# Performance work log

Hardware: AMD Instinct MI355X
Metric: run time of the kernel (lower is better)

Reference implementation:

```python
import jax, jax.numpy as jnp
import numpy as np

N = 16384          # num nodes (128 graphs x 128 turbines)
E = 262144         # edges before self loops
TURBINE_NUM = 128
D_IN = 512         # input_dim (= 2*hidden_dim1)
H1 = 256           # hidden_dim1
H2 = 256           # hidden_dim2
NEG_SLOPE = 0.2    # PyG GATConv default leaky relu slope


def _glorot(key, shape, fan_in):
    return jax.random.normal(key, shape, dtype=jnp.float32) / np.sqrt(fan_in)


def setup_inputs() -> dict:
    key = jax.random.key(0)
    ks = jax.random.split(key, 12)
    x = jax.random.normal(ks[0], (N, H2), dtype=jnp.float32)
    adj = jax.random.randint(ks[1], (2, E), 0, N, dtype=jnp.int64)
    # fc: Linear(hidden_dim2 -> hidden_dim1); stored as [in, out]
    W_fc = _glorot(ks[2], (H2, H1), H2)
    b_fc = jnp.zeros((H1,), dtype=jnp.float32)
    # gat1: GATConv(H1 -> H1, heads=2, concat)
    W1 = _glorot(ks[3], (H1, 2 * H1), H1)
    a1_src = _glorot(ks[4], (2, H1), H1)
    a1_dst = _glorot(ks[5], (2, H1), H1)
    b1 = jnp.zeros((2 * H1,), dtype=jnp.float32)
    # gat2: GATConv(D_IN -> D_IN, heads=1, concat)
    W2 = _glorot(ks[6], (D_IN, D_IN), D_IN)
    a2_src = _glorot(ks[7], (1, D_IN), D_IN)
    a2_dst = _glorot(ks[8], (1, D_IN), D_IN)
    b2 = jnp.zeros((D_IN,), dtype=jnp.float32)
    return dict(x=x, adj=adj, W_fc=W_fc, b_fc=b_fc, W1=W1, a1_src=a1_src,
                a1_dst=a1_dst, b1=b1, W2=W2, a2_src=a2_src, a2_dst=a2_dst, b2=b2)


def gat_conv(x, src, dst, W, a_src, a_dst, bias, heads, out_ch):
    """PyG GATConv (eval mode, self loops already in src/dst)."""
    n = x.shape[0]
    h = (x @ W).reshape(n, heads, out_ch)                 # [N,H,C]
    al_s = jnp.einsum('nhc,hc->nh', h, a_src)             # [N,H]
    al_d = jnp.einsum('nhc,hc->nh', h, a_dst)
    e = jax.nn.leaky_relu(al_s[src] + al_d[dst], NEG_SLOPE)  # [E,H]
    # segment softmax over incoming edges per destination node
    e_max = jax.ops.segment_max(e, dst, num_segments=n)
    e_exp = jnp.exp(e - e_max[dst])
    denom = jax.ops.segment_sum(e_exp, dst, num_segments=n)
    alpha = e_exp / (denom[dst] + 1e-16)                  # [E,H]
    msg = h[src] * alpha[:, :, None]                      # [E,H,C]
    out = jax.ops.segment_sum(msg, dst, num_segments=n)   # [N,H,C]
    return out.reshape(n, heads * out_ch) + bias


def reference(x, adj, W_fc, b_fc, W1, a1_src, a1_dst, b1, W2, a2_src, a2_dst, b2):
    # add self loops (PyG GATConv default)
    loops = jnp.arange(N, dtype=adj.dtype)
    src = jnp.concatenate([adj[0], loops])
    dst = jnp.concatenate([adj[1], loops])
    h = jax.nn.relu(x @ W_fc + b_fc)                      # fc + ReLU
    h = gat_conv(h, src, dst, W1, a1_src, a1_dst, b1, heads=2, out_ch=H1)
    h = jax.nn.relu(h)
    h = gat_conv(h, src, dst, W2, a2_src, a2_dst, b2, heads=1, out_ch=D_IN)
    y = jax.nn.relu(h)
    return y.reshape(-1, TURBINE_NUM, y.shape[1])         # [128,128,512]
```

## Files before the change

kernel.cpp:

```cpp
#include <hip/hip_runtime.h>

#define N_NODES 16384
#define N_EDGES 262144
#define E_TOT   (N_EDGES + N_NODES)
#define NEG_SLOPE 0.2f

typedef __attribute__((ext_vector_type(8))) short short8;
typedef __attribute__((ext_vector_type(4))) float floatx4;
typedef __attribute__((ext_vector_type(4))) int intx4;

__device__ __forceinline__ float bf2f(ushort u) {
    return __uint_as_float(((unsigned)u) << 16);
}
__device__ __forceinline__ ushort f2bf(float f) {
    unsigned u = __float_as_uint(f);
    u += 0x7fffu + ((u >> 16) & 1u);
    return (ushort)(u >> 16);
}
__device__ __forceinline__ float leaky(float x) {
    return x > 0.f ? x : NEG_SLOPE * x;
}

#define PREP_CAST   524288
#define PREP_T0     (PREP_CAST)
#define PREP_T1     (PREP_T0 + 65536)
#define PREP_T2     (PREP_T1 + 131072)
#define PREP_Z      (PREP_T2 + 262144)
#define PREP_TOT    (PREP_Z + 4096)

__global__ __launch_bounds__(256) void k_prep(const float* __restrict__ x,
                                              ushort* __restrict__ xb,
                                              const float* __restrict__ Wfc,
                                              ushort* __restrict__ WfcT,
                                              const float* __restrict__ W1,
                                              ushort* __restrict__ W1T,
                                              const float* __restrict__ W2,
                                              ushort* __restrict__ W2T,
                                              int* __restrict__ counts) {
    int idx = blockIdx.x * 256 + threadIdx.x;
    if (idx < PREP_CAST) {
        floatx4 v0 = *(const floatx4*)(x + (size_t)idx * 8);
        floatx4 v1 = *(const floatx4*)(x + (size_t)idx * 8 + 4);
        short8 r;
        r[0] = (short)f2bf(v0[0]); r[1] = (short)f2bf(v0[1]);
        r[2] = (short)f2bf(v0[2]); r[3] = (short)f2bf(v0[3]);
        r[4] = (short)f2bf(v1[0]); r[5] = (short)f2bf(v1[1]);
        r[6] = (short)f2bf(v1[2]); r[7] = (short)f2bf(v1[3]);
        *(short8*)(xb + (size_t)idx * 8) = r;
    } else if (idx < PREP_T1) {
        int t = idx - PREP_T0;
        int k = t >> 8, n = t & 255;
        WfcT[n * 256 + k] = f2bf(Wfc[t]);
    } else if (idx < PREP_T2) {
        int t = idx - PREP_T1;
        int k = t >> 9, n = t & 511;
        W1T[n * 256 + k] = f2bf(W1[t]);
    } else if (idx < PREP_Z) {
        int t = idx - PREP_T2;
        int k = t >> 9, n = t & 511;
        W2T[n * 512 + k] = f2bf(W2[t]);
    } else if (idx < PREP_TOT) {
        int t = idx - PREP_Z;
        *(intx4*)(counts + t * 4) = (intx4){0, 0, 0, 0};
    }
}

__global__ __launch_bounds__(256) void k_hist(const int* __restrict__ adj,
                                              int* __restrict__ counts) {
    int e = blockIdx.x * 256 + threadIdx.x;
    if (e < E_TOT) {
        int d = (e < N_EDGES) ? adj[N_EDGES + e] : (e - N_EDGES);
        atomicAdd(&counts[d], 1);
    }
}

__global__ __launch_bounds__(1024) void k_scan(const int* __restrict__ counts,
                                               int* __restrict__ offs,
                                               int* __restrict__ cursor) {
    __shared__ int wsum[16];
    int t = threadIdx.x, lane = t & 63, w = t >> 6;
    int local[16];
    int tot = 0;
#pragma unroll
    for (int i = 0; i < 16; i++) {
        local[i] = tot;
        tot += counts[t * 16 + i];
    }
    int incl = tot;
#pragma unroll
    for (int d = 1; d < 64; d <<= 1) {
        int v = __shfl_up(incl, d, 64);
        if (lane >= d) incl += v;
    }
    if (lane == 63) wsum[w] = incl;
    __syncthreads();
    if (w == 0) {
        int v = (lane < 16) ? wsum[lane] : 0;
#pragma unroll
        for (int d = 1; d < 16; d <<= 1) {
            int u = __shfl_up(v, d, 64);
            if (lane >= d) v += u;
        }
        if (lane < 16) wsum[lane] = v;
    }
    __syncthreads();
    int base = ((w == 0) ? 0 : wsum[w - 1]) + incl - tot;
#pragma unroll
    for (int i = 0; i < 16; i++) {
        int o = base + local[i];
        offs[t * 16 + i] = o;
        cursor[t * 16 + i] = o;
    }
    if (t == 1023) offs[N_NODES] = wsum[15];
}

__global__ __launch_bounds__(256) void k_scatter(const int* __restrict__ adj,
                                                 int* __restrict__ cursor,
                                                 int* __restrict__ esrc) {
    int e = blockIdx.x * 256 + threadIdx.x;
    if (e < E_TOT) {
        int s, d;
        if (e < N_EDGES) { s = adj[e]; d = adj[N_EDGES + e]; }
        else             { s = e - N_EDGES; d = s; }
        int pos = atomicAdd(&cursor[d], 1);
        esrc[pos] = s;
    }
}

#define GM 128
#define GN 128
#define GK 64
#define LDK2 72

__global__ __launch_bounds__(256) void gemm128(const ushort* __restrict__ A,
                                               const ushort* __restrict__ BT,
                                               const float* __restrict__ bias,
                                               ushort* __restrict__ C,
                                               int M, int Nc, int K, int relu) {
    __shared__ ushort As[GM * LDK2];
    __shared__ ushort Bs[GN * LDK2];
    int tid = threadIdx.x, wave = tid >> 6, lane = tid & 63;
    int quad = lane >> 4, l16 = lane & 15;
    int bm = blockIdx.x * GM, bn = blockIdx.y * GN;
    int wm = (wave & 1) * 64, wn = (wave >> 1) * 64;

    floatx4 acc[4][4];
#pragma unroll
    for (int mi = 0; mi < 4; mi++)
#pragma unroll
        for (int ni = 0; ni < 4; ni++)
            acc[mi][ni] = (floatx4){0.f, 0.f, 0.f, 0.f};

    for (int kb = 0; kb < K; kb += GK) {
        short8 av[4], bv[4];
#pragma unroll
        for (int t = 0; t < 4; t++) {
            int ci = tid + 256 * t;
            int row = ci >> 3, col = (ci & 7) * 8;
            av[t] = *(const short8*)(A + (size_t)(bm + row) * K + kb + col);
            bv[t] = *(const short8*)(BT + (size_t)(bn + row) * K + kb + col);
        }
        __syncthreads();
#pragma unroll
        for (int t = 0; t < 4; t++) {
            int ci = tid + 256 * t;
            int row = ci >> 3, col = (ci & 7) * 8;
            *(short8*)&As[row * LDK2 + col] = av[t];
            *(short8*)&Bs[row * LDK2 + col] = bv[t];
        }
        __syncthreads();

#pragma unroll
        for (int kk = 0; kk < GK; kk += 32) {
            short8 af[4], bf[4];
#pragma unroll
            for (int mi = 0; mi < 4; mi++)
                af[mi] = *(const short8*)&As[(wm + mi * 16 + l16) * LDK2 + kk + quad * 8];
#pragma unroll
            for (int ni = 0; ni < 4; ni++)
                bf[ni] = *(const short8*)&Bs[(wn + ni * 16 + l16) * LDK2 + kk + quad * 8];
#pragma unroll
            for (int mi = 0; mi < 4; mi++)
#pragma unroll
                for (int ni = 0; ni < 4; ni++)
                    acc[mi][ni] = __builtin_amdgcn_mfma_f32_16x16x32_bf16(
                        af[mi], bf[ni], acc[mi][ni], 0, 0, 0);
        }
    }

#pragma unroll
    for (int mi = 0; mi < 4; mi++) {
        int row = bm + wm + mi * 16 + quad * 4;
#pragma unroll
        for (int ni = 0; ni < 4; ni++) {
            int col = bn + wn + ni * 16 + l16;
            float bv = bias ? bias[col] : 0.f;
#pragma unroll
            for (int i = 0; i < 4; i++) {
                float v = acc[mi][ni][i] + bv;
                if (relu) v = fmaxf(v, 0.f);
                C[(size_t)(row + i) * Nc + col] = f2bf(v);
            }
        }
    }
}

__global__ __launch_bounds__(256) void k_dots(const ushort* __restrict__ h,
                                              const float* __restrict__ asrc,
                                              const float* __restrict__ adst,
                                              float* __restrict__ als,
                                              float* __restrict__ ald,
                                              int heads) {
    int wave = threadIdx.x >> 6, lane = threadIdx.x & 63;
    int n = blockIdx.x * 4 + wave;
    const ushort* hr = h + (size_t)n * 512;
    int c = lane * 8;
    short8 hv = *(const short8*)(hr + c);
    floatx4 s0 = *(const floatx4*)(asrc + c);
    floatx4 s1 = *(const floatx4*)(asrc + c + 4);
    floatx4 d0 = *(const floatx4*)(adst + c);
    floatx4 d1 = *(const floatx4*)(adst + c + 4);
    float ps = 0.f, pd = 0.f;
#pragma unroll
    for (int j = 0; j < 4; j++) {
        float hf0 = bf2f((ushort)hv[j]);
        float hf1 = bf2f((ushort)hv[j + 4]);
        ps += hf0 * s0[j] + hf1 * s1[j];
        pd += hf0 * d0[j] + hf1 * d1[j];
    }
    int w = (heads == 2) ? 32 : 64;
    for (int m = 1; m < w; m <<= 1) {
        ps += __shfl_xor(ps, m, 64);
        pd += __shfl_xor(pd, m, 64);
    }
    if (heads == 2) {
        if (lane == 0)  { als[n * 2]     = ps; ald[n * 2]     = pd; }
        if (lane == 32) { als[n * 2 + 1] = ps; ald[n * 2 + 1] = pd; }
    } else {
        if (lane == 0)  { als[n] = ps; ald[n] = pd; }
    }
}

__global__ __launch_bounds__(256) void k_agg(const ushort* __restrict__ h,
                                             const float* __restrict__ als,
                                             const float* __restrict__ ald,
                                             const int* __restrict__ offs,
                                             const int* __restrict__ esrc,
                                             const float* __restrict__ bias,
                                             ushort* __restrict__ outb,
                                             float* __restrict__ outf,
                                             int heads) {
    int wave = threadIdx.x >> 6, lane = threadIdx.x & 63;
    int n = blockIdx.x * 4 + wave;
    int base = offs[n];
    int deg  = offs[n + 1] - base;

    int myhead = (heads == 2) ? (lane >> 5) : 0;
    int c = (heads == 2) ? (myhead * 256 + (lane & 31) * 8) : lane * 8;

    float aldh0 = ald[n * heads];
    float aldh1 = (heads == 2) ? ald[n * heads + 1] : 0.f;

    float m0 = -1e30f, m1 = -1e30f;
    for (int cb = 0; cb < deg; cb += 64) {
        int i = cb + lane;
        if (i < deg) {
            int s = esrc[base + i];
            m0 = fmaxf(m0, leaky(als[s * heads] + aldh0));
            if (heads == 2) m1 = fmaxf(m1, leaky(als[s * 2 + 1] + aldh1));
        }
    }
#pragma unroll
    for (int msk = 1; msk < 64; msk <<= 1) {
        m0 = fmaxf(m0, __shfl_xor(m0, msk, 64));
        m1 = fmaxf(m1, __shfl_xor(m1, msk, 64));
    }

    float s0 = 0.f, s1 = 0.f;
    for (int cb = 0; cb < deg; cb += 64) {
        int i = cb + lane;
        if (i < deg) {
            int s = esrc[base + i];
            s0 += __expf(leaky(als[s * heads] + aldh0) - m0);
            if (heads == 2) s1 += __expf(leaky(als[s * 2 + 1] + aldh1) - m1);
        }
    }
#pragma unroll
    for (int msk = 1; msk < 64; msk <<= 1) {
        s0 += __shfl_xor(s0, msk, 64);
        s1 += __shfl_xor(s1, msk, 64);
    }
    float inv0 = 1.f / (s0 + 1e-16f);
    float inv1 = 1.f / (s1 + 1e-16f);

    float acc[8];
#pragma unroll
    for (int q = 0; q < 8; q++) acc[q] = 0.f;
    const ushort* hc = h + c;

    for (int cb = 0; cb < deg; cb += 64) {
        int i = cb + lane;
        int sv = 0;
        float p0 = 0.f, p1 = 0.f;
        if (i < deg) {
            sv = esrc[base + i];
            p0 = __expf(leaky(als[sv * heads] + aldh0) - m0) * inv0;
            if (heads == 2) p1 = __expf(leaky(als[sv * 2 + 1] + aldh1) - m1) * inv1;
        }
        int cnt = min(64, deg - cb);
        int j = 0;
        for (; j + 4 <= cnt; j += 4) {
            int sj0 = __shfl(sv, j, 64);
            int sj1 = __shfl(sv, j + 1, 64);
            int sj2 = __shfl(sv, j + 2, 64);
            int sj3 = __shfl(sv, j + 3, 64);
            float a00 = __shfl(p0, j, 64),     a01 = __shfl(p1, j, 64);
            float a10 = __shfl(p0, j + 1, 64), a11 = __shfl(p1, j + 1, 64);
            float a20 = __shfl(p0, j + 2, 64), a21 = __shfl(p1, j + 2, 64);
            float a30 = __shfl(p0, j + 3, 64), a31 = __shfl(p1, j + 3, 64);
            float al0 = myhead ? a01 : a00;
            float al1 = myhead ? a11 : a10;
            float al2 = myhead ? a21 : a20;
            float al3 = myhead ? a31 : a30;
            short8 h0v = *(const short8*)(hc + (size_t)sj0 * 512);
            short8 h1v = *(const short8*)(hc + (size_t)sj1 * 512);
            short8 h2v = *(const short8*)(hc + (size_t)sj2 * 512);
            short8 h3v = *(const short8*)(hc + (size_t)sj3 * 512);
#pragma unroll
            for (int q = 0; q < 8; q++) {
                acc[q] += al0 * bf2f((ushort)h0v[q]);
                acc[q] += al1 * bf2f((ushort)h1v[q]);
                acc[q] += al2 * bf2f((ushort)h2v[q]);
                acc[q] += al3 * bf2f((ushort)h3v[q]);
            }
        }
        for (; j < cnt; j++) {
            int s = __shfl(sv, j, 64);
            float a0 = __shfl(p0, j, 64), a1 = __shfl(p1, j, 64);
            float al = myhead ? a1 : a0;
            short8 hv = *(const short8*)(hc + (size_t)s * 512);
#pragma unroll
            for (int q = 0; q < 8; q++) acc[q] += al * bf2f((ushort)hv[q]);
        }
    }

    float v[8];
#pragma unroll
    for (int q = 0; q < 8; q++) v[q] = fmaxf(acc[q] + bias[c + q], 0.f);
    if (outf) {
        float* op = outf + (size_t)n * 512 + c;
        *(floatx4*)op       = (floatx4){v[0], v[1], v[2], v[3]};
        *(floatx4*)(op + 4) = (floatx4){v[4], v[5], v[6], v[7]};
    } else {
        short8 r;
#pragma unroll
        for (int q = 0; q < 8; q++) r[q] = (short)f2bf(v[q]);
        *(short8*)(outb + (size_t)n * 512 + c) = r;
    }
}

extern "C" void kernel_launch(void* const* d_in, const int* in_sizes, int n_in,
                              void* d_out, int out_size, void* d_ws, size_t ws_size,
                              hipStream_t stream) {
    const float* x   = (const float*)d_in[0];
    const int*   adj = (const int*)d_in[1];
    const float* Wfc = (const float*)d_in[2];
    const float* bfc = (const float*)d_in[3];
    const float* W1  = (const float*)d_in[4];
    const float* a1s = (const float*)d_in[5];
    const float* a1d = (const float*)d_in[6];
    const float* b1  = (const float*)d_in[7];
    const float* W2  = (const float*)d_in[8];
    const float* a2s = (const float*)d_in[9];
    const float* a2d = (const float*)d_in[10];
    const float* b2  = (const float*)d_in[11];
    float* out = (float*)d_out;

    char* ws = (char*)d_ws;
    size_t off = 0;
    auto alloc = [&](size_t bytes) -> void* {
        void* p = ws + off;
        off += (bytes + 255) & ~(size_t)255;
        return p;
    };
    ushort* xb   = (ushort*)alloc((size_t)N_NODES * 256 * 2);
    ushort* h0b  = (ushort*)alloc((size_t)N_NODES * 256 * 2);
    ushort* h1b  = (ushort*)alloc((size_t)N_NODES * 512 * 2);
    ushort* g1b  = (ushort*)alloc((size_t)N_NODES * 512 * 2);
    int* counts  = (int*)alloc(N_NODES * 4);
    int* offs    = (int*)alloc((N_NODES + 1) * 4);
    int* cursor  = (int*)alloc(N_NODES * 4);
    int* esrc    = (int*)alloc(E_TOT * 4);
    ushort* WfcT = (ushort*)alloc(256 * 256 * 2);
    ushort* W1T  = (ushort*)alloc(512 * 256 * 2);
    ushort* W2T  = (ushort*)alloc(512 * 512 * 2);
    float* als1  = (float*)alloc(N_NODES * 2 * 4);
    float* ald1  = (float*)alloc(N_NODES * 2 * 4);
    float* als2  = (float*)alloc(N_NODES * 4);
    float* ald2  = (float*)alloc(N_NODES * 4);

    k_prep<<<PREP_TOT / 256, 256, 0, stream>>>(x, xb, Wfc, WfcT, W1, W1T, W2, W2T,
                                               counts);

    k_hist<<<(E_TOT + 255) / 256, 256, 0, stream>>>(adj, counts);
    k_scan<<<1, 1024, 0, stream>>>(counts, offs, cursor);
    k_scatter<<<(E_TOT + 255) / 256, 256, 0, stream>>>(adj, cursor, esrc);

    gemm128<<<dim3(N_NODES / GM, 256 / GN), 256, 0, stream>>>(xb, WfcT, bfc, h0b,
                                                              N_NODES, 256, 256, 1);
    gemm128<<<dim3(N_NODES / GM, 512 / GN), 256, 0, stream>>>(h0b, W1T, nullptr, h1b,
                                                              N_NODES, 512, 256, 0);
    k_dots<<<N_NODES / 4, 256, 0, stream>>>(h1b, a1s, a1d, als1, ald1, 2);
    k_agg<<<N_NODES / 4, 256, 0, stream>>>(h1b, als1, ald1, offs, esrc, b1,
                                           g1b, nullptr, 2);

    gemm128<<<dim3(N_NODES / GM, 512 / GN), 256, 0, stream>>>(g1b, W2T, nullptr, h1b,
                                                              N_NODES, 512, 512, 0);
    k_dots<<<N_NODES / 4, 256, 0, stream>>>(h1b, a2s, a2d, als2, ald2, 1);
    k_agg<<<N_NODES / 4, 256, 0, stream>>>(h1b, als2, ald2, offs, esrc, b2,
                                           nullptr, out, 1);
}
```

Baseline: 263.1 us.

## Split GAT aggregation across two waves per node and use direct-to-LDS GEMM loads

The aggregation kernel now assigns two waves to each destination node. Each wave gathers alternating edges, and the partial sums are combined through shared memory, which increases memory-level parallelism for the gather. The GEMM replaces register-staged global-to-LDS copies with global_load_lds into an unpadded tile and adds a trailing barrier. The cost is that the softmax max and sum passes are duplicated per wave, and the unpadded LDS layout may cause bank conflicts.

```diff
diff --git a/kernel.cpp b/kernel.cpp
--- a/kernel.cpp
+++ b/kernel.cpp
@@ -19,6 +19,12 @@
 }
 __device__ __forceinline__ float leaky(float x) {
     return x > 0.f ? x : NEG_SLOPE * x;
+}
+
+__device__ __forceinline__ void load_lds16(const void* g, void* l) {
+    __builtin_amdgcn_global_load_lds(
+        (const __attribute__((address_space(1))) unsigned int*)g,
+        (__attribute__((address_space(3))) unsigned int*)l, 16, 0, 0);
 }
 
 #define PREP_CAST   524288
@@ -130,15 +136,14 @@
 #define GM 128
 #define GN 128
 #define GK 64
-#define LDK2 72
 
 __global__ __launch_bounds__(256) void gemm128(const ushort* __restrict__ A,
                                                const ushort* __restrict__ BT,
                                                const float* __restrict__ bias,
                                                ushort* __restrict__ C,
                                                int M, int Nc, int K, int relu) {
-    __shared__ ushort As[GM * LDK2];
-    __shared__ ushort Bs[GN * LDK2];
+    __shared__ ushort As[GM * GK];
+    __shared__ ushort Bs[GN * GK];
     int tid = threadIdx.x, wave = tid >> 6, lane = tid & 63;
     int quad = lane >> 4, l16 = lane & 15;
     int bm = blockIdx.x * GM, bn = blockIdx.y * GN;
@@ -151,22 +156,18 @@
         for (int ni = 0; ni < 4; ni++)
             acc[mi][ni] = (floatx4){0.f, 0.f, 0.f, 0.f};
 
+    int lrow = lane >> 3;
+    int lcol = (lane & 7) * 8;
+    const ushort* pA = A + (size_t)(bm + wave * 32 + lrow) * K + lcol;
+    const ushort* pB = BT + (size_t)(bn + wave * 32 + lrow) * K + lcol;
+    ushort* lA = &As[(wave * 32) * GK];
+    ushort* lB = &Bs[(wave * 32) * GK];
+
     for (int kb = 0; kb < K; kb += GK) {
-        short8 av[4], bv[4];
 #pragma unroll
         for (int t = 0; t < 4; t++) {
-            int ci = tid + 256 * t;
-            int row = ci >> 3, col = (ci & 7) * 8;
-            av[t] = *(const short8*)(A + (size_t)(bm + row) * K + kb + col);
-            bv[t] = *(const short8*)(BT + (size_t)(bn + row) * K + kb + col);
-        }
-        __syncthreads();
-#pragma unroll
-        for (int t = 0; t < 4; t++) {
-            int ci = tid + 256 * t;
-            int row = ci >> 3, col = (ci & 7) * 8;
-            *(short8*)&As[row * LDK2 + col] = av[t];
-            *(short8*)&Bs[row * LDK2 + col] = bv[t];
+            load_lds16(pA + (size_t)(t * 8) * K + kb, lA + t * 8 * GK);
+            load_lds16(pB + (size_t)(t * 8) * K + kb, lB + t * 8 * GK);
         }
         __syncthreads();
 
@@ -175,10 +176,10 @@
             short8 af[4], bf[4];
 #pragma unroll
             for (int mi = 0; mi < 4; mi++)
-                af[mi] = *(const short8*)&As[(wm + mi * 16 + l16) * LDK2 + kk + quad * 8];
+                af[mi] = *(const short8*)&As[(wm + mi * 16 + l16) * GK + kk + quad * 8];
 #pragma unroll
             for (int ni = 0; ni < 4; ni++)
-                bf[ni] = *(const short8*)&Bs[(wn + ni * 16 + l16) * LDK2 + kk + quad * 8];
+                bf[ni] = *(const short8*)&Bs[(wn + ni * 16 + l16) * GK + kk + quad * 8];
 #pragma unroll
             for (int mi = 0; mi < 4; mi++)
 #pragma unroll
@@ -186,6 +187,7 @@
                     acc[mi][ni] = __builtin_amdgcn_mfma_f32_16x16x32_bf16(
                         af[mi], bf[ni], acc[mi][ni], 0, 0, 0);
         }
+        __syncthreads();
     }
 
 #pragma unroll
@@ -250,8 +252,11 @@
                                              ushort* __restrict__ outb,
                                              float* __restrict__ outf,
                                              int heads) {
+    __shared__ float sPart[2][512];
     int wave = threadIdx.x >> 6, lane = threadIdx.x & 63;
-    int n = blockIdx.x * 4 + wave;
+    int nib = wave >> 1;
+    int sub = wave & 1;
+    int n = blockIdx.x * 2 + nib;
     int base = offs[n];
     int deg  = offs[n + 1] - base;
 
@@ -298,18 +303,19 @@
     for (int q = 0; q < 8; q++) acc[q] = 0.f;
     const ushort* hc = h + c;
 
-    for (int cb = 0; cb < deg; cb += 64) {
-        int i = cb + lane;
+    for (int cb = 0; cb < deg; cb += 128) {
+        int ei = cb + lane * 2 + sub;
         int sv = 0;
         float p0 = 0.f, p1 = 0.f;
-        if (i < deg) {
-            sv = esrc[base + i];
+        if (ei < deg) {
+            sv = esrc[base + ei];
             p0 = __expf(leaky(als[sv * heads] + aldh0) - m0) * inv0;
             if (heads == 2) p1 = __expf(leaky(als[sv * 2 + 1] + aldh1) - m1) * inv1;
         }
-        int cnt = min(64, deg - cb);
+        int cnt = min(128, deg - cb);
+        int nw = (cnt > sub) ? ((cnt - sub + 1) >> 1) : 0;
         int j = 0;
-        for (; j + 4 <= cnt; j += 4) {
+        for (; j + 4 <= nw; j += 4) {
             int sj0 = __shfl(sv, j, 64);
             int sj1 = __shfl(sv, j + 1, 64);
             int sj2 = __shfl(sv, j + 2, 64);
@@ -334,7 +340,7 @@
                 acc[q] += al3 * bf2f((ushort)h3v[q]);
             }
         }
-        for (; j < cnt; j++) {
+        for (; j < nw; j++) {
             int s = __shfl(sv, j, 64);
             float a0 = __shfl(p0, j, 64), a1 = __shfl(p1, j, 64);
             float al = myhead ? a1 : a0;
@@ -344,18 +350,26 @@
         }
     }
 
-    float v[8];
-#pragma unroll
-    for (int q = 0; q < 8; q++) v[q] = fmaxf(acc[q] + bias[c + q], 0.f);
-    if (outf) {
-        float* op = outf + (size_t)n * 512 + c;
-        *(floatx4*)op       = (floatx4){v[0], v[1], v[2], v[3]};
-        *(floatx4*)(op + 4) = (floatx4){v[4], v[5], v[6], v[7]};
-    } else {
-        short8 r;
-#pragma unroll
-        for (int q = 0; q < 8; q++) r[q] = (short)f2bf(v[q]);
-        *(short8*)(outb + (size_t)n * 512 + c) = r;
+    if (sub == 1) {
+#pragma unroll
+        for (int q = 0; q < 8; q++) sPart[nib][c + q] = acc[q];
+    }
+    __syncthreads();
+    if (sub == 0) {
+        float v[8];
+#pragma unroll
+        for (int q = 0; q < 8; q++)
+            v[q] = fmaxf(acc[q] + sPart[nib][c + q] + bias[c + q], 0.f);
+        if (outf) {
+            float* op = outf + (size_t)n * 512 + c;
+            *(floatx4*)op       = (floatx4){v[0], v[1], v[2], v[3]};
+            *(floatx4*)(op + 4) = (floatx4){v[4], v[5], v[6], v[7]};
+        } else {
+            short8 r;
+#pragma unroll
+            for (int q = 0; q < 8; q++) r[q] = (short)f2bf(v[q]);
+            *(short8*)(outb + (size_t)n * 512 + c) = r;
+        }
     }
 }
 
@@ -411,12 +425,12 @@
     gemm128<<<dim3(N_NODES / GM, 512 / GN), 256, 0, stream>>>(h0b, W1T, nullptr, h1b,
                                                               N_NODES, 512, 256, 0);
     k_dots<<<N_NODES / 4, 256, 0, stream>>>(h1b, a1s, a1d, als1, ald1, 2);
-    k_agg<<<N_NODES / 4, 256, 0, stream>>>(h1b, als1, ald1, offs, esrc, b1,
+    k_agg<<<N_NODES / 2, 256, 0, stream>>>(h1b, als1, ald1, offs, esrc, b1,
                                            g1b, nullptr, 2);
 
     gemm128<<<dim3(N_NODES / GM, 512 / GN), 256, 0, stream>>>(g1b, W2T, nullptr, h1b,
                                                               N_NODES, 512, 512, 0);
     k_dots<<<N_NODES / 4, 256, 0, stream>>>(h1b, a2s, a2d, als2, ald2, 1);
-    k_agg<<<N_NODES / 4, 256, 0, stream>>>(h1b, als2, ald2, offs, esrc, b2,
+    k_agg<<<N_NODES / 2, 256, 0, stream>>>(h1b, als2, ald2, offs, esrc, b2,
                                            nullptr, out, 1);
 }
```

After: 271.3 us. +3.1%, slower.
